# Kernel optimization log

Measured on AMD Instinct MI355X. Metric: run time of the kernel, lower is better.

## Reference

```python
import jax, jax.numpy as jnp
import numpy as np

N_NODES = 50000
HEADS1 = 4
NEG_SLOPE = 0.2
EPS = 1e-16


def gat_conv(x, edge_index, W, att_src, att_dst, bias, heads, out_ch, concat):
    # edge_index: [2, E] with self-loops already appended by caller
    src, dst = edge_index[0], edge_index[1]
    N = x.shape[0]
    h = (x @ W).reshape(N, heads, out_ch)                      # [N, H, C]
    a_src = jnp.sum(h * att_src, axis=-1)                      # [N, H]
    a_dst = jnp.sum(h * att_dst, axis=-1)                      # [N, H]
    e = a_src[src] + a_dst[dst]                                # [E, H]
    e = jnp.where(e > 0, e, NEG_SLOPE * e)                     # leaky_relu
    m = jax.ops.segment_max(e, dst, num_segments=N)            # [N, H]
    alpha = jnp.exp(e - m[dst])                                # [E, H]
    denom = jax.ops.segment_sum(alpha, dst, num_segments=N)    # [N, H]
    alpha = alpha / (denom[dst] + EPS)                         # [E, H]
    msg = alpha[:, :, None] * h[src]                           # [E, H, C]
    out = jax.ops.segment_sum(msg, dst, num_segments=N)        # [N, H, C]
    if concat:
        out = out.reshape(N, heads * out_ch)
    else:
        out = out.mean(axis=1)
    return out + bias, alpha


def setup_inputs() -> dict:
    key = jax.random.key(0)
    ks = jax.random.split(key, 12)
    N, F, H, heads, C, E = N_NODES, 256, 64, HEADS1, 40, 800000
    g = 0.1
    return {
        "x": jax.random.normal(ks[0], (N, F), dtype=jnp.float32),
        "edge_index": jax.random.randint(ks[1], (2, E), 0, N, dtype=jnp.int32),
        "W1": jax.random.normal(ks[2], (F, heads * H), dtype=jnp.float32) * g,
        "att_src1": jax.random.normal(ks[3], (heads, H), dtype=jnp.float32) * g,
        "att_dst1": jax.random.normal(ks[4], (heads, H), dtype=jnp.float32) * g,
        "b1": jnp.zeros((heads * H,), dtype=jnp.float32),
        "W2": jax.random.normal(ks[5], (heads * H, C), dtype=jnp.float32) * g,
        "att_src2": jax.random.normal(ks[6], (1, C), dtype=jnp.float32) * g,
        "att_dst2": jax.random.normal(ks[7], (1, C), dtype=jnp.float32) * g,
        "b2": jnp.zeros((C,), dtype=jnp.float32),
    }


def reference(x, edge_index, W1, att_src1, att_dst1, b1, W2, att_src2, att_dst2, b2):
    N = x.shape[0]
    # add self-loops (PyG GATConv default)
    loops = jnp.arange(N, dtype=edge_index.dtype)
    ei = jnp.concatenate([edge_index, jnp.stack([loops, loops])], axis=1)
    # dropout is identity in eval mode
    h1, alpha = gat_conv(x, ei, W1, att_src1, att_dst1, b1,
                         HEADS1, W1.shape[1] // HEADS1, concat=True)
    h1 = jax.nn.elu(h1)
    h2, _ = gat_conv(h1, ei, W2, att_src2, att_dst2, b2,
                     1, W2.shape[1], concat=False)
    return jax.nn.log_softmax(h2, axis=1), alpha
```

## Files before the change

### kernel.cpp

```cpp
#include <hip/hip_runtime.h>
#include <math.h>

#define N_NODES 50000
#define HC1 256
#define H1 4
#define C2 40
#define C2P 64
#define E0 800000
#define ET 850000
#define NEG_SLOPE 0.2f
#define EPS_A 1e-16f

typedef __bf16 bf16x8 __attribute__((ext_vector_type(8)));
typedef float f32x4 __attribute__((ext_vector_type(4)));
typedef unsigned short u16x8 __attribute__((ext_vector_type(8)));


__device__ inline unsigned short f2bf(float f) {
    unsigned u = __float_as_uint(f);
    return (unsigned short)((u + 0x7FFFu + ((u >> 16) & 1u)) >> 16);
}
__device__ inline float bf_lo(unsigned q) { return __uint_as_float(q << 16); }
__device__ inline float bf_hi(unsigned q) { return __uint_as_float(q & 0xFFFF0000u); }


__device__ inline int edge_src(const int* __restrict__ ei, int e) {
    return (e < E0) ? ei[e] : (e - E0);
}
__device__ inline int edge_dst(const int* __restrict__ ei, int e) {
    return (e < E0) ? ei[E0 + e] : (e - E0);
}

__device__ inline void acc8(float ac[8], float A, uint4 q) {
    ac[0] += A * bf_lo(q.x); ac[1] += A * bf_hi(q.x);
    ac[2] += A * bf_lo(q.y); ac[3] += A * bf_hi(q.y);
    ac[4] += A * bf_lo(q.z); ac[5] += A * bf_hi(q.z);
    ac[6] += A * bf_lo(q.w); ac[7] += A * bf_hi(q.w);
}

__device__ inline float leaky(float v) { return v > 0.f ? v : NEG_SLOPE * v; }


#define CV_X 3200000
#define CV_W1 65536
#define CV_W2 16384
#define CV_TOT (CV_X + CV_W1 + CV_W2 + ET)

__global__ void convert_all_kernel(const float* __restrict__ x,
                                   const float* __restrict__ W1,
                                   const float* __restrict__ W2,
                                   const int* __restrict__ ei,
                                   ushort4* __restrict__ xbf,
                                   unsigned short* __restrict__ w1t,
                                   unsigned short* __restrict__ w2t,
                                   int* __restrict__ deg) {
    int tid = blockIdx.x * blockDim.x + threadIdx.x;
    if (tid < CV_X) {
        float4 v = ((const float4*)x)[tid];
        ushort4 w;
        w.x = f2bf(v.x); w.y = f2bf(v.y); w.z = f2bf(v.z); w.w = f2bf(v.w);
        xbf[tid] = w;
    } else if (tid < CV_X + CV_W1) {
        int i = tid - CV_X;
        int n = i >> 8, k = i & 255;
        w1t[i] = f2bf(W1[k * 256 + n]);
    } else if (tid < CV_X + CV_W1 + CV_W2) {
        int i = tid - CV_X - CV_W1;
        int n = i >> 8, k = i & 255;
        w2t[i] = (n < C2) ? f2bf(W2[k * C2 + n]) : (unsigned short)0;
    } else if (tid < CV_TOT) {
        int e = tid - CV_X - CV_W1 - CV_W2;
        atomicAdd(&deg[edge_dst(ei, e)], 1);
    }
}


__global__ __launch_bounds__(256) void scan_block_kernel(const int* __restrict__ deg,
                                                         int* __restrict__ excl,
                                                         int* __restrict__ bsum) {
    __shared__ int tmp[256];
    int t = threadIdx.x;
    int i = blockIdx.x * 256 + t;
    int v = (i < N_NODES) ? deg[i] : 0;
    tmp[t] = v;
    __syncthreads();
#pragma unroll
    for (int o = 1; o < 256; o <<= 1) {
        int x = (t >= o) ? tmp[t - o] : 0;
        __syncthreads();
        tmp[t] += x;
        __syncthreads();
    }
    if (i < N_NODES) excl[i] = tmp[t] - v;
    if (t == 255) bsum[blockIdx.x] = tmp[255];
}

#define NSCAN_B 196

__global__ __launch_bounds__(256) void scan_top_kernel(int* __restrict__ bsum) {
    __shared__ int tmp[256];
    int t = threadIdx.x;
    int v = (t < NSCAN_B) ? bsum[t] : 0;
    tmp[t] = v;
    __syncthreads();
#pragma unroll
    for (int o = 1; o < 256; o <<= 1) {
        int x = (t >= o) ? tmp[t - o] : 0;
        __syncthreads();
        tmp[t] += x;
        __syncthreads();
    }
    if (t < NSCAN_B) bsum[t] = tmp[t] - v;
}

__global__ __launch_bounds__(256) void scan_add_kernel(int* __restrict__ offsets,
                                                       int* __restrict__ cursor,
                                                       const int* __restrict__ bsum) {
    int i = blockIdx.x * 256 + threadIdx.x;
    if (i < N_NODES) {
        int v = offsets[i] + bsum[blockIdx.x];
        offsets[i] = v;
        cursor[i] = v;
    }
    if (i == 0) offsets[N_NODES] = ET;
}

__global__ void scatter_kernel(const int* __restrict__ ei, int* __restrict__ cursor,
                               int2* __restrict__ csr_es) {
    int e = blockIdx.x * blockDim.x + threadIdx.x;
    if (e >= ET) return;
    int d = edge_dst(ei, e);
    int pos = atomicAdd(&cursor[d], 1);
    csr_es[pos] = make_int2(e, edge_src(ei, e));
}


#define GEMM_STAGE(k0v, bufv)                                                     \
    _Pragma("unroll")                                                             \
    for (int i = 0; i < TBM / 64; ++i) {                                          \
        int idx = t + i * 256;                                                    \
        int row = idx >> 2, seg = idx & 3;                                        \
        u16x8 v = {};                                                             \
        if (bm + row < M)                                                         \
            v = *(const u16x8*)(Abf + (size_t)(bm + row) * 256 + (k0v) + seg * 8);\
        *(u16x8*)&As[bufv][row * LDK + seg * 8] = v;                              \
    }                                                                             \
    _Pragma("unroll")                                                             \
    for (int i = 0; i < TBN / 64; ++i) {                                          \
        int idx = t + i * 256;                                                    \
        int row = idx >> 2, seg = idx & 3;                                        \
        u16x8 v = *(const u16x8*)(Bt + (size_t)(bn + row) * 256 + (k0v) + seg * 8);\
        *(u16x8*)&Bs[bufv][row * LDK + seg * 8] = v;                              \
    }

template <int TBM, int TBN, int WROWS, int WCOLS>
__global__ __launch_bounds__(256) void gemm_mfma_kernel(const unsigned short* __restrict__ Abf,
                                                        const unsigned short* __restrict__ Bt,
                                                        unsigned short* __restrict__ Cbf,
                                                        const float* __restrict__ att_s,
                                                        const float* __restrict__ att_d,
                                                        float* __restrict__ a_src_o,
                                                        float* __restrict__ a_dst_o,
                                                        int M, int Nc, int attN, int hstride) {
    static_assert(TBM == WROWS * 64 && TBN == WCOLS * 64, "tile");
    constexpr int LDK = 40;
    __shared__ alignas(16) unsigned short As[2][TBM * LDK];
    __shared__ alignas(16) unsigned short Bs[2][TBN * LDK];
    const int t = threadIdx.x;
    const int lane = t & 63;
    const int w = t >> 6;
    const int quad = lane >> 4;
    const int l16 = lane & 15;
    const int wm = (w / WCOLS) * 64;
    const int wn = (w % WCOLS) * 64;
    const int bm = blockIdx.x * TBM;
    const int bn = blockIdx.y * TBN;

    f32x4 acc[4][4] = {};

    GEMM_STAGE(0, 0);
    int cur = 0;
    for (int k0 = 0; k0 < 256; k0 += 32) {
        __syncthreads();
        if (k0 + 32 < 256) { GEMM_STAGE(k0 + 32, cur ^ 1); }

        bf16x8 af[4], bfr[4];
#pragma unroll
        for (int mi = 0; mi < 4; ++mi)
            af[mi] = *(const bf16x8*)&As[cur][(wm + mi * 16 + l16) * LDK + quad * 8];
#pragma unroll
        for (int ni = 0; ni < 4; ++ni)
            bfr[ni] = *(const bf16x8*)&Bs[cur][(wn + ni * 16 + l16) * LDK + quad * 8];
#pragma unroll
        for (int mi = 0; mi < 4; ++mi)
#pragma unroll
            for (int ni = 0; ni < 4; ++ni)
                acc[mi][ni] = __builtin_amdgcn_mfma_f32_16x16x32_bf16(
                    af[mi], bfr[ni], acc[mi][ni], 0, 0, 0);
        cur ^= 1;
    }

#pragma unroll
    for (int mi = 0; mi < 4; ++mi)
#pragma unroll
        for (int ni = 0; ni < 4; ++ni)
#pragma unroll
            for (int r = 0; r < 4; ++r) {
                int row = bm + wm + mi * 16 + quad * 4 + r;
                int col = bn + wn + ni * 16 + l16;
                if (row < M)
                    Cbf[(size_t)row * Nc + col] = f2bf(acc[mi][ni][r]);
            }

    float asc[4], adc[4];
#pragma unroll
    for (int ni = 0; ni < 4; ++ni) {
        int col = bn + wn + ni * 16 + l16;
        bool valid = col < attN;
        asc[ni] = valid ? att_s[col] : 0.f;
        adc[ni] = valid ? att_d[col] : 0.f;
    }
    float vs[16], vd[16];
#pragma unroll
    for (int mi = 0; mi < 4; ++mi)
#pragma unroll
        for (int r = 0; r < 4; ++r) {
            float s = 0.f, dd = 0.f;
#pragma unroll
            for (int ni = 0; ni < 4; ++ni) {
                s += acc[mi][ni][r] * asc[ni];
                dd += acc[mi][ni][r] * adc[ni];
            }
            vs[mi * 4 + r] = s;
            vd[mi * 4 + r] = dd;
        }
#pragma unroll
    for (int k = 0; k < 4; ++k) {
        const int o = 1 << k;
        const int b = (l16 >> k) & 1;
#pragma unroll
        for (int j = 0; j < (8 >> k); ++j) {
            float lo = vs[2 * j], hi = vs[2 * j + 1];
            float keep = b ? hi : lo, send = b ? lo : hi;
            vs[j] = keep + __shfl_xor(send, o);
            lo = vd[2 * j]; hi = vd[2 * j + 1];
            keep = b ? hi : lo; send = b ? lo : hi;
            vd[j] = keep + __shfl_xor(send, o);
        }
    }
    {
        int mi = l16 >> 2, r = l16 & 3;
        int row = bm + wm + mi * 16 + quad * 4 + r;
        int head = (bn + wn) >> 6;
        if (row < M) {
            a_src_o[(size_t)row * hstride + head] = vs[0];
            a_dst_o[(size_t)row * hstride + head] = vd[0];
        }
    }
}


#define L1_LOADQ(q, jb)                                                         \
    _Pragma("unroll")                                                           \
    for (int k = 0; k < 4; ++k) {                                               \
        int s_ = __shfl(esy, shbase + (jb) + k);                                \
        q[k] = *(const uint4*)&h1bf[(unsigned)s_ * 128u + 4u * li];             \
    }

#define L1_FMAQ(q, jb)                                                          \
    _Pragma("unroll")                                                           \
    for (int k = 0; k < 4; ++k) {                                               \
        float A_ = aw[4 * ((jb) + k) + headc];                                  \
        acc8(ac, A_, q[k]);                                                     \
    }

__global__ __launch_bounds__(256) void l1_fused_kernel(const int* __restrict__ off,
                                                       const int2* __restrict__ csr_es,
                                                       const float4* __restrict__ a_src4,
                                                       const float4* __restrict__ a_dst4,
                                                       const unsigned* __restrict__ h1bf,
                                                       const float* __restrict__ b1,
                                                       float4* __restrict__ alpha_out4,
                                                       unsigned* __restrict__ out1bf) {
    __shared__ int    s_w[4][2][32];
    __shared__ float4 p_w[4][2][32];
    int t = threadIdx.x;
    int w = t >> 6, lane = t & 63;
    int half = lane >> 5, li = lane & 31;
    int shbase = half << 5;
    int d = blockIdx.x * 8 + w * 2 + half;
    int beg = off[d], end = off[d + 1];
    int deg = end - beg;
    int nch = (deg + 31) >> 5;
    int cnt0 = min(deg, 32);
    bool act0 = li < cnt0;
    float4 ad4 = a_dst4[d];
    int headc = li >> 3;

    float ac[8] = {};
    float4 sum = make_float4(0.f, 0.f, 0.f, 0.f);
    float4 mx = make_float4(-INFINITY, -INFINITY, -INFINITY, -INFINITY);
    int2 es0 = make_int2(0, 0);
    float4 p0 = make_float4(0.f, 0.f, 0.f, 0.f);

    const float* aw = (const float*)&p_w[w][half][0];
    const int*   sw = &s_w[w][half][0];

    if (nch == 1) {
        float4 l0 = make_float4(-INFINITY, -INFINITY, -INFINITY, -INFINITY);
        float4 as4 = make_float4(0.f, 0.f, 0.f, 0.f);
        if (act0) {
            es0 = csr_es[beg + li];
            as4 = a_src4[es0.y];
        }
        int esy = es0.y;
        const int B = (cnt0 + 3) >> 2;

        uint4 qa[4], qb[4];
        L1_LOADQ(qa, 0);
        if (B > 1) { L1_LOADQ(qb, 4); }

        if (act0) {
            l0.x = leaky(as4.x + ad4.x);
            l0.y = leaky(as4.y + ad4.y);
            l0.z = leaky(as4.z + ad4.z);
            l0.w = leaky(as4.w + ad4.w);
        }
        mx = l0;
#pragma unroll
        for (int o = 1; o <= 16; o <<= 1) {
            mx.x = fmaxf(mx.x, __shfl_xor(mx.x, o));
            mx.y = fmaxf(mx.y, __shfl_xor(mx.y, o));
            mx.z = fmaxf(mx.z, __shfl_xor(mx.z, o));
            mx.w = fmaxf(mx.w, __shfl_xor(mx.w, o));
        }
        p0.x = __expf(l0.x - mx.x);
        p0.y = __expf(l0.y - mx.y);
        p0.z = __expf(l0.z - mx.z);
        p0.w = __expf(l0.w - mx.w);
        p_w[w][half][li] = p0;
        sum = p0;

        int i = 0;
        for (; i + 2 <= B; i += 2) {
            L1_FMAQ(qa, i * 4);
            if (i + 2 < B) { L1_LOADQ(qa, (i + 2) * 4); }
            L1_FMAQ(qb, i * 4 + 4);
            if (i + 3 < B) { L1_LOADQ(qb, (i + 3) * 4); }
        }
        if (i < B) { L1_FMAQ(qa, i * 4); }
    } else {
        for (int cc = 0; cc < nch; ++cc) {
            int idx = beg + cc * 32 + li;
            if (idx < end) {
                int2 es = csr_es[idx];
                float4 as4 = a_src4[es.y];
                mx.x = fmaxf(mx.x, leaky(as4.x + ad4.x));
                mx.y = fmaxf(mx.y, leaky(as4.y + ad4.y));
                mx.z = fmaxf(mx.z, leaky(as4.z + ad4.z));
                mx.w = fmaxf(mx.w, leaky(as4.w + ad4.w));
            }
        }
#pragma unroll
        for (int o = 1; o <= 16; o <<= 1) {
            mx.x = fmaxf(mx.x, __shfl_xor(mx.x, o));
            mx.y = fmaxf(mx.y, __shfl_xor(mx.y, o));
            mx.z = fmaxf(mx.z, __shfl_xor(mx.z, o));
            mx.w = fmaxf(mx.w, __shfl_xor(mx.w, o));
        }
        for (int cc = 0; cc < nch; ++cc) {
            int idx = beg + cc * 32 + li;
            if (idx < end) {
                int2 es = csr_es[idx];
                float4 as4 = a_src4[es.y];
                sum.x += __expf(leaky(as4.x + ad4.x) - mx.x);
                sum.y += __expf(leaky(as4.y + ad4.y) - mx.y);
                sum.z += __expf(leaky(as4.z + ad4.z) - mx.z);
                sum.w += __expf(leaky(as4.w + ad4.w) - mx.w);
            }
        }
    }

#pragma unroll
    for (int o = 1; o <= 16; o <<= 1) {
        sum.x += __shfl_xor(sum.x, o);
        sum.y += __shfl_xor(sum.y, o);
        sum.z += __shfl_xor(sum.z, o);
        sum.w += __shfl_xor(sum.w, o);
    }
    float4 inv;
    inv.x = 1.f / (sum.x + EPS_A); inv.y = 1.f / (sum.y + EPS_A);
    inv.z = 1.f / (sum.z + EPS_A); inv.w = 1.f / (sum.w + EPS_A);
    float invh = (headc == 0) ? inv.x : (headc == 1) ? inv.y
               : (headc == 2) ? inv.z : inv.w;

    if (nch == 1) {
        if (act0) {
            float4 al0;
            al0.x = p0.x * inv.x; al0.y = p0.y * inv.y;
            al0.z = p0.z * inv.z; al0.w = p0.w * inv.w;
            alpha_out4[es0.x] = al0;
        }
    } else {
        for (int cc = 0; cc < nch; ++cc) {
            int idx = beg + cc * 32 + li;
            int cnt = min(32, deg - cc * 32);
            if (idx < end) {
                int2 es = csr_es[idx];
                float4 as4 = a_src4[es.y];
                float4 p;
                p.x = __expf(leaky(as4.x + ad4.x) - mx.x);
                p.y = __expf(leaky(as4.y + ad4.y) - mx.y);
                p.z = __expf(leaky(as4.z + ad4.z) - mx.z);
                p.w = __expf(leaky(as4.w + ad4.w) - mx.w);
                float4 al;
                al.x = p.x * inv.x; al.y = p.y * inv.y;
                al.z = p.z * inv.z; al.w = p.w * inv.w;
                alpha_out4[es.x] = al;
                s_w[w][half][li] = es.y;
                p_w[w][half][li] = p;
            }
            for (int j = 0; j < cnt; ++j) {
                int s = sw[j];
                float A = aw[4 * j + headc];
                uint4 q = *(const uint4*)&h1bf[(unsigned)s * 128u + 4u * li];
                acc8(ac, A, q);
            }
        }
    }

#pragma unroll
    for (int c = 0; c < 8; ++c) ac[c] *= invh;

    float4 bb0 = *(const float4*)&b1[8 * li];
    float4 bb1 = *(const float4*)&b1[8 * li + 4];
    float v0 = ac[0] + bb0.x, v1 = ac[1] + bb0.y;
    float v2 = ac[2] + bb0.z, v3 = ac[3] + bb0.w;
    float v4 = ac[4] + bb1.x, v5 = ac[5] + bb1.y;
    float v6 = ac[6] + bb1.z, v7 = ac[7] + bb1.w;
    v0 = v0 > 0.f ? v0 : __expf(v0) - 1.f;
    v1 = v1 > 0.f ? v1 : __expf(v1) - 1.f;
    v2 = v2 > 0.f ? v2 : __expf(v2) - 1.f;
    v3 = v3 > 0.f ? v3 : __expf(v3) - 1.f;
    v4 = v4 > 0.f ? v4 : __expf(v4) - 1.f;
    v5 = v5 > 0.f ? v5 : __expf(v5) - 1.f;
    v6 = v6 > 0.f ? v6 : __expf(v6) - 1.f;
    v7 = v7 > 0.f ? v7 : __expf(v7) - 1.f;
    uint4 qo;
    qo.x = ((unsigned)f2bf(v1) << 16) | (unsigned)f2bf(v0);
    qo.y = ((unsigned)f2bf(v3) << 16) | (unsigned)f2bf(v2);
    qo.z = ((unsigned)f2bf(v5) << 16) | (unsigned)f2bf(v4);
    qo.w = ((unsigned)f2bf(v7) << 16) | (unsigned)f2bf(v6);
    *(uint4*)&out1bf[(size_t)d * 128 + 4 * li] = qo;
}


#define L2_LOADQ(q, jb)                                                         \
    _Pragma("unroll")                                                           \
    for (int k = 0; k < 4; ++k) {                                               \
        int s_ = __shfl(s0, shbase + (jb) + k);                                 \
        q[k] = h2bf[(unsigned)s_ * 32u + li];                                   \
    }

#define L2_FMAQ(q, jb)                                                          \
    _Pragma("unroll")                                                           \
    for (int k = 0; k < 4; ++k) {                                               \
        float A_ = __shfl(p0, shbase + (jb) + k);                               \
        acc0 += A_ * bf_lo(q[k]);                                               \
        acc1 += A_ * bf_hi(q[k]);                                               \
    }

__global__ __launch_bounds__(256) void l2_fused_kernel(const int* __restrict__ off,
                                                       const int2* __restrict__ csr_es,
                                                       const float* __restrict__ a_src,
                                                       const float* __restrict__ a_dst,
                                                       const unsigned* __restrict__ h2bf,
                                                       const float* __restrict__ b2,
                                                       float* __restrict__ out) {
    __shared__ uint2 sp_w[4][2][32];
    int t = threadIdx.x;
    int w = t >> 6, lane = t & 63;
    int half = lane >> 5, li = lane & 31;
    int shbase = half << 5;
    int d = blockIdx.x * 8 + w * 2 + half;
    int beg = off[d], end = off[d + 1];
    int deg = end - beg;
    float ad = a_dst[d];
    int nch = (deg + 31) >> 5;
    int cnt0 = min(deg, 32);
    bool act0 = li < cnt0;

    float sum = 0.f, acc0 = 0.f, acc1 = 0.f;
    float p0 = 0.f;

    if (nch == 1) {
        float el0 = -INFINITY; int s0 = 0;
        if (act0) {
            int2 es = csr_es[beg + li];
            s0 = es.y;
            el0 = leaky(a_src[s0] + ad);
        }
        const int B = (cnt0 + 3) >> 2;
        unsigned q[8][4];
#pragma unroll
        for (int i = 0; i < 8; ++i)
            if (i < B) { L2_LOADQ(q[i], i * 4); }

        float mx = el0;
#pragma unroll
        for (int o = 1; o <= 16; o <<= 1) mx = fmaxf(mx, __shfl_xor(mx, o));
        p0 = __expf(el0 - mx);
        sum = p0;

#pragma unroll
        for (int i = 0; i < 8; ++i)
            if (i < B) { L2_FMAQ(q[i], i * 4); }
    } else {
        float mx = -INFINITY;
        for (int cc = 0; cc < nch; ++cc) {
            int idx = beg + cc * 32 + li;
            if (idx < end) {
                int2 es = csr_es[idx];
                mx = fmaxf(mx, leaky(a_src[es.y] + ad));
            }
        }
#pragma unroll
        for (int o = 1; o <= 16; o <<= 1) mx = fmaxf(mx, __shfl_xor(mx, o));
        for (int cc = 0; cc < nch; ++cc) {
            int idx = beg + cc * 32 + li;
            int cnt = min(32, deg - cc * 32);
            if (idx < end) {
                int2 es = csr_es[idx];
                float el = leaky(a_src[es.y] + ad);
                float p = __expf(el - mx);
                sum += p;
                sp_w[w][half][li] = make_uint2((unsigned)es.y, __float_as_uint(p));
            }
            for (int j = 0; j < cnt; ++j) {
                uint2 e0 = sp_w[w][half][j];
                float A0 = __uint_as_float(e0.y);
                unsigned qv = h2bf[e0.x * 32u + li];
                acc0 += A0 * bf_lo(qv);
                acc1 += A0 * bf_hi(qv);
            }
        }
    }

#pragma unroll
    for (int o = 1; o <= 16; o <<= 1) sum += __shfl_xor(sum, o);
    float inv = 1.f / (sum + EPS_A);
    acc0 *= inv;
    acc1 *= inv;

    bool act = li < 20;
    float v0 = act ? acc0 + b2[2 * li]     : -INFINITY;
    float v1 = act ? acc1 + b2[2 * li + 1] : -INFINITY;
    float mmx = fmaxf(v0, v1);
#pragma unroll
    for (int o = 16; o; o >>= 1) mmx = fmaxf(mmx, __shfl_xor(mmx, o));
    float ex = act ? __expf(v0 - mmx) + __expf(v1 - mmx) : 0.f;
#pragma unroll
    for (int o = 16; o; o >>= 1) ex += __shfl_xor(ex, o);
    float ls = __logf(ex);
    if (act)
        *(float2*)&out[(size_t)d * C2 + 2 * li] = make_float2(v0 - mmx - ls, v1 - mmx - ls);
}


extern "C" void kernel_launch(void* const* d_in, const int* in_sizes, int n_in,
                              void* d_out, int out_size, void* d_ws, size_t ws_size,
                              hipStream_t stream) {
    const float* x   = (const float*)d_in[0];
    const int*   ei  = (const int*)d_in[1];
    const float* W1  = (const float*)d_in[2];
    const float* as1 = (const float*)d_in[3];
    const float* ad1 = (const float*)d_in[4];
    const float* b1  = (const float*)d_in[5];
    const float* W2  = (const float*)d_in[6];
    const float* as2 = (const float*)d_in[7];
    const float* ad2 = (const float*)d_in[8];
    const float* b2  = (const float*)d_in[9];

    float* out   = (float*)d_out;
    float* alpha = out + (size_t)N_NODES * C2;

    unsigned* u32    = (unsigned*)d_ws;
    unsigned* h1bf   = u32;
    unsigned* xbf    = h1bf + 6400000;
    unsigned* h2bf   = xbf + 6400000;
    unsigned* w1t    = h2bf + 1600000;
    unsigned* w2t    = w1t + 32768;
    float* a_src1    = (float*)(w2t + 8192);
    float* a_dst1    = a_src1 + 200000;
    float* a_src2    = a_dst1 + 200000;
    float* a_dst2    = a_src2 + 50000;
    int*   deg       = (int*)(a_dst2 + 50000);
    int*   offs      = deg + 50000;
    int*   cursor    = offs + 50001;
    int*   bsum      = cursor + 50000;
    int2*  csr_es    = (int2*)(bsum + 257);
    unsigned* out1bf = xbf;

    const int TB = 256;
    const int EB = (ET + TB - 1) / TB;

    hipMemsetAsync(deg, 0, (size_t)N_NODES * sizeof(int), stream);

    convert_all_kernel<<<(CV_TOT + TB - 1) / TB, TB, 0, stream>>>(
        x, W1, W2, ei, (ushort4*)xbf, (unsigned short*)w1t, (unsigned short*)w2t, deg);

    scan_block_kernel<<<NSCAN_B, TB, 0, stream>>>(deg, offs, bsum);
    scan_top_kernel<<<1, TB, 0, stream>>>(bsum);
    scan_add_kernel<<<NSCAN_B, TB, 0, stream>>>(offs, cursor, bsum);
    scatter_kernel<<<EB, TB, 0, stream>>>(ei, cursor, csr_es);

    gemm_mfma_kernel<128, 128, 2, 2><<<dim3((N_NODES + 127) / 128, 2), TB, 0, stream>>>(
        (const unsigned short*)xbf, (const unsigned short*)w1t, (unsigned short*)h1bf,
        as1, ad1, a_src1, a_dst1, N_NODES, HC1, 256, H1);
    l1_fused_kernel<<<N_NODES / 8, TB, 0, stream>>>(offs, csr_es,
                                                    (const float4*)a_src1,
                                                    (const float4*)a_dst1,
                                                    h1bf, b1, (float4*)alpha, out1bf);

    gemm_mfma_kernel<256, 64, 4, 1><<<dim3((N_NODES + 255) / 256, 1), TB, 0, stream>>>(
        (const unsigned short*)out1bf, (const unsigned short*)w2t, (unsigned short*)h2bf,
        as2, ad2, a_src2, a_dst2, N_NODES, C2P, C2, 1);
    l2_fused_kernel<<<N_NODES / 8, TB, 0, stream>>>(offs, csr_es, a_src2, a_dst2,
                                                    h2bf, b2, out);
}
```

Before: 356.4 us.

## Fuse x fp32-to-bf16 conversion into layer-1 GEMM tile loads

Drops the separate pass that converted x to bf16 in the convert kernel. The layer-1 GEMM now reads fp32 x directly and converts to bf16 while staging A tiles into shared memory. This removes a write and re-read of a 25.6MB bf16 copy. The layer-1 tile also changes from 128x128 over two column blocks to 64x256 in one, so each x row is read once rather than twice, at the cost of more global load bandwidth per tile and conversion ALU work inside the GEMM.

```diff
diff --git a/kernel.cpp b/kernel.cpp
--- a/kernel.cpp
+++ b/kernel.cpp
@@ -41,35 +41,26 @@
 __device__ inline float leaky(float v) { return v > 0.f ? v : NEG_SLOPE * v; }
 
 
-#define CV_X 3200000
 #define CV_W1 65536
 #define CV_W2 16384
-#define CV_TOT (CV_X + CV_W1 + CV_W2 + ET)
-
-__global__ void convert_all_kernel(const float* __restrict__ x,
-                                   const float* __restrict__ W1,
+#define CV_TOT (CV_W1 + CV_W2 + ET)
+
+__global__ void convert_all_kernel(const float* __restrict__ W1,
                                    const float* __restrict__ W2,
                                    const int* __restrict__ ei,
-                                   ushort4* __restrict__ xbf,
                                    unsigned short* __restrict__ w1t,
                                    unsigned short* __restrict__ w2t,
                                    int* __restrict__ deg) {
     int tid = blockIdx.x * blockDim.x + threadIdx.x;
-    if (tid < CV_X) {
-        float4 v = ((const float4*)x)[tid];
-        ushort4 w;
-        w.x = f2bf(v.x); w.y = f2bf(v.y); w.z = f2bf(v.z); w.w = f2bf(v.w);
-        xbf[tid] = w;
-    } else if (tid < CV_X + CV_W1) {
-        int i = tid - CV_X;
-        int n = i >> 8, k = i & 255;
-        w1t[i] = f2bf(W1[k * 256 + n]);
-    } else if (tid < CV_X + CV_W1 + CV_W2) {
-        int i = tid - CV_X - CV_W1;
+    if (tid < CV_W1) {
+        int n = tid >> 8, k = tid & 255;
+        w1t[tid] = f2bf(W1[k * 256 + n]);
+    } else if (tid < CV_W1 + CV_W2) {
+        int i = tid - CV_W1;
         int n = i >> 8, k = i & 255;
         w2t[i] = (n < C2) ? f2bf(W2[k * C2 + n]) : (unsigned short)0;
     } else if (tid < CV_TOT) {
-        int e = tid - CV_X - CV_W1 - CV_W2;
+        int e = tid - CV_W1 - CV_W2;
         atomicAdd(&deg[edge_dst(ei, e)], 1);
     }
 }
@@ -141,20 +132,32 @@
         int idx = t + i * 256;                                                    \
         int row = idx >> 2, seg = idx & 3;                                        \
         u16x8 v = {};                                                             \
-        if (bm + row < M)                                                         \
-            v = *(const u16x8*)(Abf + (size_t)(bm + row) * 256 + (k0v) + seg * 8);\
+        if (bm + row < M) {                                                       \
+            if constexpr (AF32) {                                                 \
+                const float* sp = Af32 + (size_t)(bm + row) * 256 + (k0v) + seg * 8; \
+                float4 f0 = *(const float4*)sp;                                   \
+                float4 f1 = *(const float4*)(sp + 4);                             \
+                v[0] = f2bf(f0.x); v[1] = f2bf(f0.y);                             \
+                v[2] = f2bf(f0.z); v[3] = f2bf(f0.w);                             \
+                v[4] = f2bf(f1.x); v[5] = f2bf(f1.y);                             \
+                v[6] = f2bf(f1.z); v[7] = f2bf(f1.w);                             \
+            } else {                                                              \
+                v = *(const u16x8*)(Abf + (size_t)(bm + row) * 256 + (k0v) + seg * 8); \
+            }                                                                     \
+        }                                                                         \
         *(u16x8*)&As[bufv][row * LDK + seg * 8] = v;                              \
     }                                                                             \
     _Pragma("unroll")                                                             \
     for (int i = 0; i < TBN / 64; ++i) {                                          \
         int idx = t + i * 256;                                                    \
         int row = idx >> 2, seg = idx & 3;                                        \
-        u16x8 v = *(const u16x8*)(Bt + (size_t)(bn + row) * 256 + (k0v) + seg * 8);\
+        u16x8 v = *(const u16x8*)(Bt + (size_t)(bn + row) * 256 + (k0v) + seg * 8); \
         *(u16x8*)&Bs[bufv][row * LDK + seg * 8] = v;                              \
     }
 
-template <int TBM, int TBN, int WROWS, int WCOLS>
+template <int TBM, int TBN, int WROWS, int WCOLS, bool AF32>
 __global__ __launch_bounds__(256) void gemm_mfma_kernel(const unsigned short* __restrict__ Abf,
+                                                        const float* __restrict__ Af32,
                                                         const unsigned short* __restrict__ Bt,
                                                         unsigned short* __restrict__ Cbf,
                                                         const float* __restrict__ att_s,
@@ -586,8 +589,8 @@
 
     unsigned* u32    = (unsigned*)d_ws;
     unsigned* h1bf   = u32;
-    unsigned* xbf    = h1bf + 6400000;
-    unsigned* h2bf   = xbf + 6400000;
+    unsigned* out1bf = h1bf + 6400000;
+    unsigned* h2bf   = out1bf + 6400000;
     unsigned* w1t    = h2bf + 1600000;
     unsigned* w2t    = w1t + 32768;
     float* a_src1    = (float*)(w2t + 8192);
@@ -599,7 +602,6 @@
     int*   cursor    = offs + 50001;
     int*   bsum      = cursor + 50000;
     int2*  csr_es    = (int2*)(bsum + 257);
-    unsigned* out1bf = xbf;
 
     const int TB = 256;
     const int EB = (ET + TB - 1) / TB;
@@ -607,24 +609,24 @@
     hipMemsetAsync(deg, 0, (size_t)N_NODES * sizeof(int), stream);
 
     convert_all_kernel<<<(CV_TOT + TB - 1) / TB, TB, 0, stream>>>(
-        x, W1, W2, ei, (ushort4*)xbf, (unsigned short*)w1t, (unsigned short*)w2t, deg);
+        W1, W2, ei, (unsigned short*)w1t, (unsigned short*)w2t, deg);
 
     scan_block_kernel<<<NSCAN_B, TB, 0, stream>>>(deg, offs, bsum);
     scan_top_kernel<<<1, TB, 0, stream>>>(bsum);
     scan_add_kernel<<<NSCAN_B, TB, 0, stream>>>(offs, cursor, bsum);
     scatter_kernel<<<EB, TB, 0, stream>>>(ei, cursor, csr_es);
 
-    gemm_mfma_kernel<128, 128, 2, 2><<<dim3((N_NODES + 127) / 128, 2), TB, 0, stream>>>(
-        (const unsigned short*)xbf, (const unsigned short*)w1t, (unsigned short*)h1bf,
+    gemm_mfma_kernel<64, 256, 1, 4, true><<<dim3((N_NODES + 63) / 64, 1), TB, 0, stream>>>(
+        nullptr, x, (const unsigned short*)w1t, (unsigned short*)h1bf,
         as1, ad1, a_src1, a_dst1, N_NODES, HC1, 256, H1);
     l1_fused_kernel<<<N_NODES / 8, TB, 0, stream>>>(offs, csr_es,
                                                     (const float4*)a_src1,
                                                     (const float4*)a_dst1,
                                                     h1bf, b1, (float4*)alpha, out1bf);
 
-    gemm_mfma_kernel<256, 64, 4, 1><<<dim3((N_NODES + 255) / 256, 1), TB, 0, stream>>>(
-        (const unsigned short*)out1bf, (const unsigned short*)w2t, (unsigned short*)h2bf,
-        as2, ad2, a_src2, a_dst2, N_NODES, C2P, C2, 1);
+    gemm_mfma_kernel<256, 64, 4, 1, false><<<dim3((N_NODES + 255) / 256, 1), TB, 0, stream>>>(
+        (const unsigned short*)out1bf, nullptr, (const unsigned short*)w2t,
+        (unsigned short*)h2bf, as2, ad2, a_src2, a_dst2, N_NODES, C2P, C2, 1);
     l2_fused_kernel<<<N_NODES / 8, TB, 0, stream>>>(offs, csr_es, a_src2, a_dst2,
                                                     h2bf, b2, out);
 }
```

Result: no change. 351.7 us (-1.3%).
